# Kernel optimization log

Measured on AMD Instinct MI355X. Metric: run time of the kernel, lower is better.

Reference implementation:

```python
import jax, jax.numpy as jnp
import numpy as np

P = 16          # patch size
NUM_HEADS = 8
WINDOW = 64     # window_size from SparseAttention(window_size=64)


def _layer_norm(x, w, b, eps=1e-5):
    mu = jnp.mean(x, axis=-1, keepdims=True)
    var = jnp.var(x, axis=-1, keepdims=True)
    return (x - mu) * jax.lax.rsqrt(var + eps) * w + b


def _sinusoidal_pe(num_patches, num_features, dtype):
    pos = jnp.arange(num_patches, dtype=jnp.float32)[:, None]            # [N,1]
    i = jnp.arange(0, num_features, 2, dtype=jnp.float32)                # [D/2]
    div = jnp.exp(-jnp.log(10000.0) * i / num_features)                  # [D/2]
    ang = pos * div                                                      # [N,D/2]
    pe = jnp.stack([jnp.sin(ang), jnp.cos(ang)], axis=-1).reshape(num_patches, num_features)
    return pe.astype(dtype)


def _ffn(x, w1, b1, w2, b2):
    # FeedForward: Linear -> GELU -> Linear (dropout inactive at eval)
    h = jax.nn.gelu(jnp.einsum('bnd,hd->bnh', x, w1) + b1)
    return jnp.einsum('bnh,dh->bnd', h, w2) + b2


def _windowed_attention(x, qkv_w, qkv_b, proj_w, proj_b):
    B, N, D = x.shape
    hd = D // NUM_HEADS
    qkv = jnp.einsum('bnd,ed->bne', x, qkv_w) + qkv_b                    # [B,N,3D]
    qkv = qkv.reshape(B, N, 3, NUM_HEADS, hd)
    q, k, v = qkv[:, :, 0], qkv[:, :, 1], qkv[:, :, 2]                   # [B,N,H,hd]
    nw = N // WINDOW
    # partition sequence into non-overlapping windows of 64 tokens
    q = q.reshape(B, nw, WINDOW, NUM_HEADS, hd).transpose(0, 3, 1, 2, 4)  # [B,H,nw,W,hd]
    k = k.reshape(B, nw, WINDOW, NUM_HEADS, hd).transpose(0, 3, 1, 2, 4)
    v = v.reshape(B, nw, WINDOW, NUM_HEADS, hd).transpose(0, 3, 1, 2, 4)
    scale = 1.0 / jnp.sqrt(jnp.asarray(hd, x.dtype))
    scores = jnp.einsum('bhwqd,bhwkd->bhwqk', q, k) * scale              # [B,H,nw,W,W]
    attn = jax.nn.softmax(scores, axis=-1)
    out = jnp.einsum('bhwqk,bhwkd->bhwqd', attn, v)                      # [B,H,nw,W,hd]
    out = out.transpose(0, 2, 3, 1, 4).reshape(B, N, D)
    return jnp.einsum('bnd,ed->bne', out, proj_w) + proj_b


def setup_inputs() -> dict:
    key = jax.random.key(0)
    ks = jax.random.split(key, 8)
    D, HF = 256, 1024
    s = lambda fan: 1.0 / np.sqrt(fan)
    return {
        'x': jax.random.normal(ks[0], (32, 3, 512, 512), jnp.float32),
        'conv_w': jax.random.normal(ks[1], (D, 3, P, P), jnp.float32) * s(3 * P * P),
        'conv_b': jnp.zeros((D,), jnp.float32),
        'ln_w': jnp.ones((D,), jnp.float32),
        'ln_b': jnp.zeros((D,), jnp.float32),
        'qkv_w': jax.random.normal(ks[2], (3 * D, D), jnp.float32) * s(D),
        'qkv_b': jnp.zeros((3 * D,), jnp.float32),
        'proj_w': jax.random.normal(ks[3], (D, D), jnp.float32) * s(D),
        'proj_b': jnp.zeros((D,), jnp.float32),
        'ff_w1': jax.random.normal(ks[4], (HF, D), jnp.float32) * s(D),
        'ff_b1': jnp.zeros((HF,), jnp.float32),
        'ff_w2': jax.random.normal(ks[5], (D, HF), jnp.float32) * s(HF),
        'ff_b2': jnp.zeros((D,), jnp.float32),
    }


def reference(x, conv_w, conv_b, ln_w, ln_b, qkv_w, qkv_b, proj_w, proj_b,
              ff_w1, ff_b1, ff_w2, ff_b2):
    B, C, H, W = x.shape
    D = conv_w.shape[0]
    # PatchEmbedding1: Conv2d(C, D, kernel=16, stride=16) == per-patch matmul, then LayerNorm
    nH, nW = H // P, W // P
    patches = x.reshape(B, C, nH, P, nW, P).transpose(0, 2, 4, 1, 3, 5).reshape(B, nH * nW, C * P * P)
    h = jnp.einsum('bnp,dp->bnd', patches, conv_w.reshape(D, -1)) + conv_b
    h = _layer_norm(h, ln_w, ln_b)
    # static sinusoidal position embedding
    h = h + _sinusoidal_pe(h.shape[1], D, h.dtype)
    # block 1: FFN -> sparse (windowed) attention -> residual
    identity = h
    h = _ffn(h, ff_w1, ff_b1, ff_w2, ff_b2)
    h = _windowed_attention(h, qkv_w, qkv_b, proj_w, proj_b)
    h = h + identity
    # block 2: shared FFN -> residual
    identity = h
    h = _ffn(h, ff_w1, ff_b1, ff_w2, ff_b2)
    return h + identity
```

## Files before the change

kernel.cpp:

```cpp
#include <hip/hip_runtime.h>
#include <math.h>


#define M_TOK 32768

typedef __attribute__((ext_vector_type(8))) short  short8;
typedef __attribute__((ext_vector_type(4))) float  f32x4;
typedef __attribute__((ext_vector_type(8))) unsigned short us8v;
typedef __attribute__((ext_vector_type(4))) unsigned short us4v;

__device__ __forceinline__ unsigned short f2b(float f) {
    union { float f; unsigned u; } c; c.f = f;
    unsigned r = c.u + 0x7fffu + ((c.u >> 16) & 1u);
    return (unsigned short)(r >> 16);
}
__device__ __forceinline__ float gelu_fast(float x) {
    const float c0 = 0.7978845608028654f;
    const float c1 = 0.044715f * 0.7978845608028654f;
    float z = x * (c0 + c1 * x * x);
    float e = __expf(-2.0f * z);
    return x * __builtin_amdgcn_rcpf(1.0f + e);
}
__device__ __forceinline__ void load_lds16(const unsigned short* g, void* lds) {
    __builtin_amdgcn_global_load_lds(
        (const __attribute__((address_space(1))) unsigned int*)g,
        (__attribute__((address_space(3))) unsigned int*)lds, 16, 0, 0);
}

__global__ __launch_bounds__(256) void cvt_f2b_kernel(
    const float* __restrict__ in, unsigned short* __restrict__ out, int n)
{
    int i = (blockIdx.x * 256 + threadIdx.x) * 4;
    if (i >= n) return;
    float4 v = *(const float4*)(in + i);
    us4v o;
    o[0] = f2b(v.x); o[1] = f2b(v.y); o[2] = f2b(v.z); o[3] = f2b(v.w);
    *(us4v*)(out + i) = o;
}

__global__ __launch_bounds__(256) void cvt_weights_kernel(
    const float* __restrict__ s0, const float* __restrict__ s1,
    const float* __restrict__ s2, const float* __restrict__ s3,
    const float* __restrict__ s4,
    unsigned short* __restrict__ d0, unsigned short* __restrict__ d1,
    unsigned short* __restrict__ d2, unsigned short* __restrict__ d3,
    unsigned short* __restrict__ d4)
{
    const int bid = blockIdx.x;
    const float* src; unsigned short* dst; int off;
    if      (bid < 192) { src = s0; dst = d0; off = bid; }
    else if (bid < 384) { src = s1; dst = d1; off = bid - 192; }
    else if (bid < 448) { src = s2; dst = d2; off = bid - 384; }
    else if (bid < 704) { src = s3; dst = d3; off = bid - 448; }
    else                { src = s4; dst = d4; off = bid - 704; }
    const int i = off * 1024 + threadIdx.x * 4;
    float4 v = *(const float4*)(src + i);
    us4v o;
    o[0] = f2b(v.x); o[1] = f2b(v.y); o[2] = f2b(v.z); o[3] = f2b(v.w);
    *(us4v*)(dst + i) = o;
}

__global__ __launch_bounds__(256) void pe_init_kernel(float* __restrict__ pe)
{
    const int pos = blockIdx.x;
    const int d   = threadIdx.x;
    const int ieven = d & ~1;
    float div = expf(-9.210340371976184f * (float)ieven * (1.0f / 256.0f));
    float ang = (float)pos * div;
    pe[pos * 256 + d] = (d & 1) ? cosf(ang) : sinf(ang);
}

template<bool GELU, bool RES, bool WF32, bool WB16>
__global__ __launch_bounds__(512) void mfma_gemm_kernel(
    const unsigned short* __restrict__ A, const unsigned short* __restrict__ W,
    const float* __restrict__ bias, const float* __restrict__ res,
    float* __restrict__ outF, unsigned short* __restrict__ outB,
    int M, int N, int K)
{
    __shared__ unsigned short As[2 * 128 * 64];
    __shared__ unsigned short Ws[2 * 128 * 64];

    const int t    = threadIdx.x;
    const int m0   = blockIdx.x * 128;
    const int n0   = blockIdx.y * 128;
    const int wv   = t >> 6, lane = t & 63;
    const int wr   = (wv >> 2) * 64;
    const int wc   = (wv & 3) * 32;
    const int l15  = lane & 15, quad = lane >> 4;

    f32x4 acc[4][2];
#pragma unroll
    for (int i = 0; i < 4; i++)
#pragma unroll
        for (int j = 0; j < 2; j++)
#pragma unroll
            for (int r = 0; r < 4; r++) acc[i][j][r] = 0.0f;

    const int srow = wv * 8 + (lane >> 3);
    const int skk  = (((lane & 7) ^ ((lane >> 3) & 7)) * 8);
    const unsigned short* gA = A + (size_t)(m0 + srow) * K + skk;
    const unsigned short* gW = W + (size_t)(n0 + srow) * K + skk;
    char* lA = (char*)As + wv * 1024;
    char* lW = (char*)Ws + wv * 1024;

    const int cswz = (l15 & 7) * 8;
    const int nt   = K >> 6;

#define GSTAGE(tt, BUFOFF)                                                     \
    {                                                                          \
        const int kk = (tt) << 6;                                              \
        _Pragma("unroll")                                                      \
        for (int s = 0; s < 2; s++) {                                          \
            load_lds16(gA + (size_t)(s * 64) * K + kk, lA + (BUFOFF) + s * 8192); \
            load_lds16(gW + (size_t)(s * 64) * K + kk, lW + (BUFOFF) + s * 8192); \
        }                                                                      \
    }

#define GCOMPUTE(BUFOFF)                                                       \
    {                                                                          \
        const unsigned short* Ab = (const unsigned short*)((const char*)As + (BUFOFF)); \
        const unsigned short* Wb = (const unsigned short*)((const char*)Ws + (BUFOFF)); \
        _Pragma("unroll")                                                      \
        for (int kh = 0; kh < 2; kh++) {                                       \
            const int coff = (kh * 32 + quad * 8) ^ cswz;                      \
            short8 af[4], wf[2];                                               \
            _Pragma("unroll")                                                  \
            for (int i = 0; i < 4; i++)                                        \
                af[i] = *(const short8*)&Ab[(wr + i * 16 + l15) * 64 + coff];  \
            _Pragma("unroll")                                                  \
            for (int j = 0; j < 2; j++)                                        \
                wf[j] = *(const short8*)&Wb[(wc + j * 16 + l15) * 64 + coff];  \
            _Pragma("unroll")                                                  \
            for (int i = 0; i < 4; i++)                                        \
                _Pragma("unroll")                                              \
                for (int j = 0; j < 2; j++)                                    \
                    acc[i][j] = __builtin_amdgcn_mfma_f32_16x16x32_bf16(       \
                        af[i], wf[j], acc[i][j], 0, 0, 0);                     \
        }                                                                      \
    }

    GSTAGE(0, 0);
    for (int tt = 0; tt < nt; tt += 2) {
        GSTAGE(tt + 1, 16384);
        asm volatile("s_waitcnt vmcnt(4)" ::: "memory");
        __builtin_amdgcn_s_barrier();
        __builtin_amdgcn_sched_barrier(0);
        GCOMPUTE(0);
        __builtin_amdgcn_s_barrier();
        if (tt + 2 < nt) {
            GSTAGE(tt + 2, 0);
            asm volatile("s_waitcnt vmcnt(4)" ::: "memory");
        } else {
            asm volatile("s_waitcnt vmcnt(0)" ::: "memory");
        }
        __builtin_amdgcn_s_barrier();
        __builtin_amdgcn_sched_barrier(0);
        GCOMPUTE(16384);
        __builtin_amdgcn_s_barrier();
    }
#undef GSTAGE
#undef GCOMPUTE

#pragma unroll
    for (int i = 0; i < 4; i++) {
        const int gr = m0 + wr + i * 16 + quad * 4;
#pragma unroll
        for (int j = 0; j < 2; j++) {
            const int gc = n0 + wc + j * 16 + l15;
            const float bv = bias[gc];
#pragma unroll
            for (int r = 0; r < 4; r++) {
                float v = acc[i][j][r] + bv;
                if (GELU) v = gelu_fast(v);
                if (RES)  v += res[(size_t)(gr + r) * N + gc];
                if (WF32) outF[(size_t)(gr + r) * N + gc] = v;
                if (WB16) outB[(size_t)(gr + r) * N + gc] = f2b(v);
            }
        }
    }
}

__global__ __launch_bounds__(512) void patch_mfma_kernel(
    const unsigned short* __restrict__ xb, const unsigned short* __restrict__ W,
    const float* __restrict__ bias, float* __restrict__ outF)
{
    __shared__ unsigned short As[2 * 128 * 64];
    __shared__ unsigned short Ws[2 * 128 * 64];

    const int t    = threadIdx.x;
    const int m0   = blockIdx.x * 128;
    const int n0   = blockIdx.y * 128;
    const int wv   = t >> 6, lane = t & 63;
    const int wr   = (wv >> 2) * 64;
    const int wc   = (wv & 3) * 32;
    const int l15  = lane & 15, quad = lane >> 4;

    f32x4 acc[4][2];
#pragma unroll
    for (int i = 0; i < 4; i++)
#pragma unroll
        for (int j = 0; j < 2; j++)
#pragma unroll
            for (int r = 0; r < 4; r++) acc[i][j][r] = 0.0f;

    const int srow = wv * 8 + (lane >> 3);
    const int skk  = (((lane & 7) ^ ((lane >> 3) & 7)) * 8);
    size_t xoff[2];
#pragma unroll
    for (int s = 0; s < 2; s++) {
        const int m  = m0 + s * 64 + srow;
        const int b  = m >> 10;
        const int idx = m & 1023;
        const int hh = idx >> 5, ww = idx & 31;
        xoff[s] = ((size_t)(b * 3) * 512 + (size_t)(hh * 16)) * 512 + ww * 16;
    }
    const unsigned short* gW = W + (size_t)(n0 + srow) * 768 + skk;
    char* lA = (char*)As + wv * 1024;
    char* lW = (char*)Ws + wv * 1024;

    const int cswz = (l15 & 7) * 8;

#define PSTAGE(tt, BUFOFF)                                                     \
    {                                                                          \
        const int kk = ((tt) << 6) + skk;    \
        const int c  = kk >> 8;                                                \
        const int ph = (kk >> 4) & 15;                                         \
        const int pw = kk & 15;                                                \
        const size_t koff = (size_t)c * 262144 + (size_t)ph * 512 + pw;        \
        _Pragma("unroll")                                                      \
        for (int s = 0; s < 2; s++) {                                          \
            load_lds16(xb + xoff[s] + koff, lA + (BUFOFF) + s * 8192);         \
            load_lds16(gW + (size_t)(s * 64) * 768 + ((tt) << 6),              \
                       lW + (BUFOFF) + s * 8192);                              \
        }                                                                      \
    }

#define PCOMPUTE(BUFOFF)                                                       \
    {                                                                          \
        const unsigned short* Ab = (const unsigned short*)((const char*)As + (BUFOFF)); \
        const unsigned short* Wb = (const unsigned short*)((const char*)Ws + (BUFOFF)); \
        _Pragma("unroll")                                                      \
        for (int kh = 0; kh < 2; kh++) {                                       \
            const int coff = (kh * 32 + quad * 8) ^ cswz;                      \
            short8 af[4], wf[2];                                               \
            _Pragma("unroll")                                                  \
            for (int i = 0; i < 4; i++)                                        \
                af[i] = *(const short8*)&Ab[(wr + i * 16 + l15) * 64 + coff];  \
            _Pragma("unroll")                                                  \
            for (int j = 0; j < 2; j++)                                        \
                wf[j] = *(const short8*)&Wb[(wc + j * 16 + l15) * 64 + coff];  \
            _Pragma("unroll")                                                  \
            for (int i = 0; i < 4; i++)                                        \
                _Pragma("unroll")                                              \
                for (int j = 0; j < 2; j++)                                    \
                    acc[i][j] = __builtin_amdgcn_mfma_f32_16x16x32_bf16(       \
                        af[i], wf[j], acc[i][j], 0, 0, 0);                     \
        }                                                                      \
    }

    PSTAGE(0, 0);
    for (int tt = 0; tt < 12; tt += 2) {
        PSTAGE(tt + 1, 16384);
        asm volatile("s_waitcnt vmcnt(4)" ::: "memory");
        __builtin_amdgcn_s_barrier();
        __builtin_amdgcn_sched_barrier(0);
        PCOMPUTE(0);
        __builtin_amdgcn_s_barrier();
        if (tt + 2 < 12) {
            PSTAGE(tt + 2, 0);
            asm volatile("s_waitcnt vmcnt(4)" ::: "memory");
        } else {
            asm volatile("s_waitcnt vmcnt(0)" ::: "memory");
        }
        __builtin_amdgcn_s_barrier();
        __builtin_amdgcn_sched_barrier(0);
        PCOMPUTE(16384);
        __builtin_amdgcn_s_barrier();
    }
#undef PSTAGE
#undef PCOMPUTE

#pragma unroll
    for (int i = 0; i < 4; i++) {
        const int gr = m0 + wr + i * 16 + quad * 4;
#pragma unroll
        for (int j = 0; j < 2; j++) {
            const int gc = n0 + wc + j * 16 + l15;
            const float bv = bias[gc];
#pragma unroll
            for (int r = 0; r < 4; r++)
                outF[(size_t)(gr + r) * 256 + gc] = acc[i][j][r] + bv;
        }
    }
}

__global__ __launch_bounds__(256) void ln_pe_kernel(
    const float* __restrict__ in, const float* __restrict__ w,
    const float* __restrict__ b, const float* __restrict__ pe_t,
    float* __restrict__ outF, unsigned short* __restrict__ outB)
{
    const int m = blockIdx.x;
    const int d = threadIdx.x;
    float v = in[(size_t)m * 256 + d];

    float s = v, s2 = v * v;
#pragma unroll
    for (int off = 32; off > 0; off >>= 1) {
        s  += __shfl_down(s,  off, 64);
        s2 += __shfl_down(s2, off, 64);
    }
    __shared__ float ss[4], ss2[4], stats[2];
    const int lane = d & 63, wid = d >> 6;
    if (lane == 0) { ss[wid] = s; ss2[wid] = s2; }
    __syncthreads();
    if (d == 0) {
        float a  = ss[0] + ss[1] + ss[2] + ss[3];
        float a2 = ss2[0] + ss2[1] + ss2[2] + ss2[3];
        float mean = a * (1.0f / 256.0f);
        float var  = a2 * (1.0f / 256.0f) - mean * mean;
        stats[0] = mean;
        stats[1] = rsqrtf(var + 1e-5f);
    }
    __syncthreads();
    const float mean = stats[0], rstd = stats[1];

    const int pos = m & 1023;
    float pe = pe_t[pos * 256 + d];

    float o = (v - mean) * rstd * w[d] + b[d] + pe;
    outF[(size_t)m * 256 + d] = o;
    outB[(size_t)m * 256 + d] = f2b(o);
}

__global__ __launch_bounds__(256) void attn_mfma_kernel(
    const unsigned short* __restrict__ qkv, unsigned short* __restrict__ out)
{
    __shared__ unsigned short Ps[64 * 72];
    __shared__ unsigned short Vt[32 * 72];

    const int blk = blockIdx.x;
    const int h = blk & 7;
    const int w = (blk >> 3) & 15;
    const int b = blk >> 7;
    const int m_base = b * 1024 + w * 64;

    const int t = threadIdx.x;
    const int wv = t >> 6, lane = t & 63;
    const int l15 = lane & 15, quad = lane >> 4;

    {
        const int row = t >> 2;
        const int c0  = (t & 3) * 8;
        const unsigned short* src = qkv + (size_t)(m_base + row) * 768 + 512 + h * 32 + c0;
        us8v v = *(const us8v*)src;
#pragma unroll
        for (int j = 0; j < 8; j++) Vt[(c0 + j) * 72 + row] = v[j];
    }

    short8 aq = *(const short8*)(qkv + (size_t)(m_base + wv * 16 + l15) * 768 + h * 32 + quad * 8);
    f32x4 c[4];
#pragma unroll
    for (int j = 0; j < 4; j++) {
        short8 bk = *(const short8*)(qkv + (size_t)(m_base + j * 16 + l15) * 768 + 256 + h * 32 + quad * 8);
        f32x4 z = {0.0f, 0.0f, 0.0f, 0.0f};
        c[j] = __builtin_amdgcn_mfma_f32_16x16x32_bf16(aq, bk, z, 0, 0, 0);
    }

    const float scale = 0.17677669529663687f;
    float sm[4];
#pragma unroll
    for (int r = 0; r < 4; r++) {
        float m0 = -1e30f;
#pragma unroll
        for (int j = 0; j < 4; j++) { c[j][r] *= scale; m0 = fmaxf(m0, c[j][r]); }
#pragma unroll
        for (int d = 1; d < 16; d <<= 1) m0 = fmaxf(m0, __shfl_xor(m0, d, 64));
        float s0 = 0.0f;
#pragma unroll
        for (int j = 0; j < 4; j++) { float e = __expf(c[j][r] - m0); c[j][r] = e; s0 += e; }
#pragma unroll
        for (int d = 1; d < 16; d <<= 1) s0 += __shfl_xor(s0, d, 64);
        sm[r] = __builtin_amdgcn_rcpf(s0);
    }

#pragma unroll
    for (int r = 0; r < 4; r++) {
        const int prow = wv * 16 + quad * 4 + r;
#pragma unroll
        for (int j = 0; j < 4; j++)
            Ps[prow * 72 + j * 16 + l15] = f2b(c[j][r] * sm[r]);
    }
    __syncthreads();

    short8 ap0 = *(const short8*)&Ps[(wv * 16 + l15) * 72 + quad * 8];
    short8 ap1 = *(const short8*)&Ps[(wv * 16 + l15) * 72 + 32 + quad * 8];
    f32x4 o[2];
#pragma unroll
    for (int nt = 0; nt < 2; nt++) {
        short8 bv0 = *(const short8*)&Vt[(nt * 16 + l15) * 72 + quad * 8];
        short8 bv1 = *(const short8*)&Vt[(nt * 16 + l15) * 72 + 32 + quad * 8];
        f32x4 z = {0.0f, 0.0f, 0.0f, 0.0f};
        o[nt] = __builtin_amdgcn_mfma_f32_16x16x32_bf16(ap0, bv0, z, 0, 0, 0);
        o[nt] = __builtin_amdgcn_mfma_f32_16x16x32_bf16(ap1, bv1, o[nt], 0, 0, 0);
    }

#pragma unroll
    for (int nt = 0; nt < 2; nt++) {
#pragma unroll
        for (int r = 0; r < 4; r++) {
            const int row = m_base + wv * 16 + quad * 4 + r;
            out[(size_t)row * 256 + h * 32 + nt * 16 + l15] = f2b(o[nt][r]);
        }
    }
}

extern "C" void kernel_launch(void* const* d_in, const int* in_sizes, int n_in,
                              void* d_out, int out_size, void* d_ws, size_t ws_size,
                              hipStream_t stream)
{
    const float* x      = (const float*)d_in[0];
    const float* conv_w = (const float*)d_in[1];
    const float* conv_b = (const float*)d_in[2];
    const float* ln_w   = (const float*)d_in[3];
    const float* ln_b   = (const float*)d_in[4];
    const float* qkv_w  = (const float*)d_in[5];
    const float* qkv_b  = (const float*)d_in[6];
    const float* proj_w = (const float*)d_in[7];
    const float* proj_b = (const float*)d_in[8];
    const float* ff_w1  = (const float*)d_in[9];
    const float* ff_b1  = (const float*)d_in[10];
    const float* ff_w2  = (const float*)d_in[11];
    const float* ff_b2  = (const float*)d_in[12];
    float* out = (float*)d_out;

    char* ws = (char*)d_ws;
    unsigned short* xb    = (unsigned short*)(ws);
    unsigned short* hidb  = (unsigned short*)(ws);
    float*          h0    = (float*)(ws + 67108864);
    unsigned short* qkvb  = (unsigned short*)(ws + 67108864);
    float*          pe_t  = (float*)(ws + 100663296);
    float*          h1f   = (float*)(ws + 117440512);
    unsigned short* h1b   = (unsigned short*)(ws + 150994944);
    unsigned short* aob   = (unsigned short*)(ws + 150994944);
    unsigned short* f1b   = (unsigned short*)(ws + 167772160);
    unsigned short* h2b   = (unsigned short*)(ws + 167772160);
    unsigned short* wbase = (unsigned short*)(ws + 184549376);
    unsigned short* conv_wb = wbase;
    unsigned short* qkv_wb  = wbase + 196608;
    unsigned short* proj_wb = wbase + 393216;
    unsigned short* ff_w1b  = wbase + 458752;
    unsigned short* ff_w2b  = wbase + 720896;

    const int M = M_TOK;
    dim3 blk(256);
    dim3 blk512(512);

    cvt_f2b_kernel<<<dim3(25165824 / 1024), blk, 0, stream>>>(x, xb, 25165824);
    cvt_weights_kernel<<<dim3(960), blk, 0, stream>>>(
        conv_w, qkv_w, proj_w, ff_w1, ff_w2,
        conv_wb, qkv_wb, proj_wb, ff_w1b, ff_w2b);
    pe_init_kernel<<<dim3(1024), blk, 0, stream>>>(pe_t);

    patch_mfma_kernel<<<dim3(M / 128, 2), blk512, 0, stream>>>(xb, conv_wb, conv_b, h0);
    ln_pe_kernel<<<dim3(M), blk, 0, stream>>>(h0, ln_w, ln_b, pe_t, h1f, h1b);
    mfma_gemm_kernel<true, false, false, true><<<dim3(M / 128, 8), blk512, 0, stream>>>(
        h1b, ff_w1b, ff_b1, nullptr, nullptr, hidb, M, 1024, 256);
    mfma_gemm_kernel<false, false, false, true><<<dim3(M / 128, 2), blk512, 0, stream>>>(
        hidb, ff_w2b, ff_b2, nullptr, nullptr, f1b, M, 256, 1024);
    mfma_gemm_kernel<false, false, false, true><<<dim3(M / 128, 6), blk512, 0, stream>>>(
        f1b, qkv_wb, qkv_b, nullptr, nullptr, qkvb, M, 768, 256);
    attn_mfma_kernel<<<dim3(4096), blk, 0, stream>>>(qkvb, aob);
    mfma_gemm_kernel<false, true, true, true><<<dim3(M / 128, 2), blk512, 0, stream>>>(
        aob, proj_wb, proj_b, h1f, out, h2b, M, 256, 256);
    mfma_gemm_kernel<true, false, false, true><<<dim3(M / 128, 8), blk512, 0, stream>>>(
        h2b, ff_w1b, ff_b1, nullptr, nullptr, hidb, M, 1024, 256);
    mfma_gemm_kernel<false, true, true, false><<<dim3(M / 128, 2), blk512, 0, stream>>>(
        hidb, ff_w2b, ff_b2, out, out, nullptr, M, 256, 1024);
}
```

Measured before the change: 394.3 us.

## Fuse fp32-to-bf16 input conversion into patch-embedding GEMM with full-N tile

Removes the separate kernel that converted the 100MB fp32 image to bf16. The patch GEMM now loads fp32 pixels directly through registers, converts them and writes swizzled bf16 into LDS. Each block covers all 256 output features (N=256), so every image tile is read once instead of twice. The cost is a register-staged A path in place of the direct global-to-LDS loads, more accumulators per wave, and double the weight LDS.

```diff
diff --git a/kernel.cpp b/kernel.cpp
--- a/kernel.cpp
+++ b/kernel.cpp
@@ -25,17 +25,6 @@
     __builtin_amdgcn_global_load_lds(
         (const __attribute__((address_space(1))) unsigned int*)g,
         (__attribute__((address_space(3))) unsigned int*)lds, 16, 0, 0);
-}
-
-__global__ __launch_bounds__(256) void cvt_f2b_kernel(
-    const float* __restrict__ in, unsigned short* __restrict__ out, int n)
-{
-    int i = (blockIdx.x * 256 + threadIdx.x) * 4;
-    if (i >= n) return;
-    float4 v = *(const float4*)(in + i);
-    us4v o;
-    o[0] = f2b(v.x); o[1] = f2b(v.y); o[2] = f2b(v.z); o[3] = f2b(v.w);
-    *(us4v*)(out + i) = o;
 }
 
 __global__ __launch_bounds__(256) void cvt_weights_kernel(
@@ -180,112 +169,134 @@
     }
 }
 
-__global__ __launch_bounds__(512) void patch_mfma_kernel(
-    const unsigned short* __restrict__ xb, const unsigned short* __restrict__ W,
+__global__ __launch_bounds__(512) void patch_fused_kernel(
+    const float* __restrict__ x, const unsigned short* __restrict__ W,
     const float* __restrict__ bias, float* __restrict__ outF)
 {
     __shared__ unsigned short As[2 * 128 * 64];
-    __shared__ unsigned short Ws[2 * 128 * 64];
+    __shared__ unsigned short Ws[2 * 256 * 64];
 
     const int t    = threadIdx.x;
     const int m0   = blockIdx.x * 128;
-    const int n0   = blockIdx.y * 128;
     const int wv   = t >> 6, lane = t & 63;
     const int wr   = (wv >> 2) * 64;
-    const int wc   = (wv & 3) * 32;
+    const int wc   = (wv & 3) * 64;
     const int l15  = lane & 15, quad = lane >> 4;
 
-    f32x4 acc[4][2];
+    f32x4 acc[4][4];
 #pragma unroll
     for (int i = 0; i < 4; i++)
 #pragma unroll
-        for (int j = 0; j < 2; j++)
+        for (int j = 0; j < 4; j++)
 #pragma unroll
             for (int r = 0; r < 4; r++) acc[i][j][r] = 0.0f;
 
-    const int srow = wv * 8 + (lane >> 3);
-    const int skk  = (((lane & 7) ^ ((lane >> 3) & 7)) * 8);
-    size_t xoff[2];
-#pragma unroll
-    for (int s = 0; s < 2; s++) {
-        const int m  = m0 + s * 64 + srow;
-        const int b  = m >> 10;
-        const int idx = m & 1023;
-        const int hh = idx >> 5, ww = idx & 31;
-        xoff[s] = ((size_t)(b * 3) * 512 + (size_t)(hh * 16)) * 512 + ww * 16;
-    }
-    const unsigned short* gW = W + (size_t)(n0 + srow) * 768 + skk;
-    char* lA = (char*)As + wv * 1024;
+    const int ar  = t >> 2;
+    const int ac0 = (t & 3) * 16;
+    const int am  = m0 + ar;
+    const int ab  = am >> 10;
+    const int ahh = (am >> 5) & 31;
+    const int aww = am & 31;
+    const float* axbase = x + (size_t)ab * 786432 + (size_t)ahh * 8192 + aww * 16;
+    const int alc = ac0 >> 3;
+    char* aw0 = (char*)As + ar * 128 + ((alc    ) ^ (ar & 7)) * 16;
+    char* aw1 = (char*)As + ar * 128 + ((alc + 1) ^ (ar & 7)) * 16;
+
+    const int wsrow = wv * 8 + (lane >> 3);
+    const int wskk  = (((lane & 7) ^ ((lane >> 3) & 7)) * 8);
+    const unsigned short* gW = W + (size_t)wsrow * 768 + wskk;
     char* lW = (char*)Ws + wv * 1024;
 
     const int cswz = (l15 & 7) * 8;
 
-#define PSTAGE(tt, BUFOFF)                                                     \
-    {                                                                          \
-        const int kk = ((tt) << 6) + skk;    \
-        const int c  = kk >> 8;                                                \
-        const int ph = (kk >> 4) & 15;                                         \
-        const int pw = kk & 15;                                                \
-        const size_t koff = (size_t)c * 262144 + (size_t)ph * 512 + pw;        \
+    float4 av0, av1, av2, av3;
+
+#define PA_ISSUE(tt)                                                           \
+    {                                                                          \
+        const int k0 = ((tt) << 6) + ac0;                                      \
+        const int c  = k0 >> 8;                                                \
+        const int ph = (k0 >> 4) & 15;                                         \
+        const float* s = axbase + (size_t)c * 262144 + ph * 512;               \
+        av0 = *(const float4*)(s);                                             \
+        av1 = *(const float4*)(s + 4);                                         \
+        av2 = *(const float4*)(s + 8);                                         \
+        av3 = *(const float4*)(s + 12);                                        \
+    }
+#define PA_WRITE(BUFOFF)                                                       \
+    {                                                                          \
+        us8v o0, o1;                                                           \
+        o0[0] = f2b(av0.x); o0[1] = f2b(av0.y); o0[2] = f2b(av0.z); o0[3] = f2b(av0.w); \
+        o0[4] = f2b(av1.x); o0[5] = f2b(av1.y); o0[6] = f2b(av1.z); o0[7] = f2b(av1.w); \
+        o1[0] = f2b(av2.x); o1[1] = f2b(av2.y); o1[2] = f2b(av2.z); o1[3] = f2b(av2.w); \
+        o1[4] = f2b(av3.x); o1[5] = f2b(av3.y); o1[6] = f2b(av3.z); o1[7] = f2b(av3.w); \
+        *(us8v*)(aw0 + (BUFOFF)) = o0;                                         \
+        *(us8v*)(aw1 + (BUFOFF)) = o1;                                         \
+    }
+#define PW_ISSUE(tt, BUFOFF)                                                   \
+    {                                                                          \
+        const int kk = (tt) << 6;                                              \
         _Pragma("unroll")                                                      \
-        for (int s = 0; s < 2; s++) {                                          \
-            load_lds16(xb + xoff[s] + koff, lA + (BUFOFF) + s * 8192);         \
-            load_lds16(gW + (size_t)(s * 64) * 768 + ((tt) << 6),              \
-                       lW + (BUFOFF) + s * 8192);                              \
-        }                                                                      \
-    }
-
-#define PCOMPUTE(BUFOFF)                                                       \
-    {                                                                          \
-        const unsigned short* Ab = (const unsigned short*)((const char*)As + (BUFOFF)); \
-        const unsigned short* Wb = (const unsigned short*)((const char*)Ws + (BUFOFF)); \
+        for (int s = 0; s < 4; s++)                                            \
+            load_lds16(gW + (size_t)(s * 64) * 768 + kk, lW + (BUFOFF) + s * 8192); \
+    }
+#define PCOMPUTE(AOFF, WOFF)                                                   \
+    {                                                                          \
+        const unsigned short* Ab = (const unsigned short*)((const char*)As + (AOFF)); \
+        const unsigned short* Wb = (const unsigned short*)((const char*)Ws + (WOFF)); \
         _Pragma("unroll")                                                      \
         for (int kh = 0; kh < 2; kh++) {                                       \
             const int coff = (kh * 32 + quad * 8) ^ cswz;                      \
-            short8 af[4], wf[2];                                               \
+            short8 af[4], wf[4];                                               \
             _Pragma("unroll")                                                  \
             for (int i = 0; i < 4; i++)                                        \
                 af[i] = *(const short8*)&Ab[(wr + i * 16 + l15) * 64 + coff];  \
             _Pragma("unroll")                                                  \
-            for (int j = 0; j < 2; j++)                                        \
+            for (int j = 0; j < 4; j++)                                        \
                 wf[j] = *(const short8*)&Wb[(wc + j * 16 + l15) * 64 + coff];  \
             _Pragma("unroll")                                                  \
             for (int i = 0; i < 4; i++)                                        \
                 _Pragma("unroll")                                              \
-                for (int j = 0; j < 2; j++)                                    \
+                for (int j = 0; j < 4; j++)                                    \
                     acc[i][j] = __builtin_amdgcn_mfma_f32_16x16x32_bf16(       \
                         af[i], wf[j], acc[i][j], 0, 0, 0);                     \
         }                                                                      \
     }
 
-    PSTAGE(0, 0);
-    for (int tt = 0; tt < 12; tt += 2) {
-        PSTAGE(tt + 1, 16384);
-        asm volatile("s_waitcnt vmcnt(4)" ::: "memory");
-        __builtin_amdgcn_s_barrier();
-        __builtin_amdgcn_sched_barrier(0);
-        PCOMPUTE(0);
-        __builtin_amdgcn_s_barrier();
-        if (tt + 2 < 12) {
-            PSTAGE(tt + 2, 0);
-            asm volatile("s_waitcnt vmcnt(4)" ::: "memory");
-        } else {
+    PA_ISSUE(0);
+    PW_ISSUE(0, 0);
+    asm volatile("s_waitcnt vmcnt(0)" ::: "memory");
+    PA_WRITE(0);
+    asm volatile("s_waitcnt lgkmcnt(0)" ::: "memory");
+    __builtin_amdgcn_s_barrier();
+    __builtin_amdgcn_sched_barrier(0);
+
+    for (int tt = 0; tt < 12; ++tt) {
+        const int aoff_c = (tt & 1) * 16384;
+        const int woff_c = (tt & 1) * 32768;
+        if (tt < 11) {
+            PA_ISSUE(tt + 1);
+            PW_ISSUE(tt + 1, woff_c ^ 32768);
+        }
+        PCOMPUTE(aoff_c, woff_c);
+        if (tt < 11) {
             asm volatile("s_waitcnt vmcnt(0)" ::: "memory");
-        }
-        __builtin_amdgcn_s_barrier();
-        __builtin_amdgcn_sched_barrier(0);
-        PCOMPUTE(16384);
-        __builtin_amdgcn_s_barrier();
-    }
-#undef PSTAGE
+            PA_WRITE(aoff_c ^ 16384);
+            asm volatile("s_waitcnt lgkmcnt(0)" ::: "memory");
+            __builtin_amdgcn_s_barrier();
+            __builtin_amdgcn_sched_barrier(0);
+        }
+    }
+#undef PA_ISSUE
+#undef PA_WRITE
+#undef PW_ISSUE
 #undef PCOMPUTE
 
 #pragma unroll
     for (int i = 0; i < 4; i++) {
         const int gr = m0 + wr + i * 16 + quad * 4;
 #pragma unroll
-        for (int j = 0; j < 2; j++) {
-            const int gc = n0 + wc + j * 16 + l15;
+        for (int j = 0; j < 4; j++) {
+            const int gc = wc + j * 16 + l15;
             const float bv = bias[gc];
 #pragma unroll
             for (int r = 0; r < 4; r++)
@@ -434,7 +445,6 @@
     float* out = (float*)d_out;
 
     char* ws = (char*)d_ws;
-    unsigned short* xb    = (unsigned short*)(ws);
     unsigned short* hidb  = (unsigned short*)(ws);
     float*          h0    = (float*)(ws + 67108864);
     unsigned short* qkvb  = (unsigned short*)(ws + 67108864);
@@ -455,13 +465,12 @@
     dim3 blk(256);
     dim3 blk512(512);
 
-    cvt_f2b_kernel<<<dim3(25165824 / 1024), blk, 0, stream>>>(x, xb, 25165824);
     cvt_weights_kernel<<<dim3(960), blk, 0, stream>>>(
         conv_w, qkv_w, proj_w, ff_w1, ff_w2,
         conv_wb, qkv_wb, proj_wb, ff_w1b, ff_w2b);
     pe_init_kernel<<<dim3(1024), blk, 0, stream>>>(pe_t);
 
-    patch_mfma_kernel<<<dim3(M / 128, 2), blk512, 0, stream>>>(xb, conv_wb, conv_b, h0);
+    patch_fused_kernel<<<dim3(M / 128), blk512, 0, stream>>>(x, conv_wb, conv_b, h0);
     ln_pe_kernel<<<dim3(M), blk, 0, stream>>>(h0, ln_w, ln_b, pe_t, h1f, h1b);
     mfma_gemm_kernel<true, false, false, true><<<dim3(M / 128, 8), blk512, 0, stream>>>(
         h1b, ff_w1b, ff_b1, nullptr, nullptr, hidb, M, 1024, 256);
```

Result: no change. 389.0 us (-1.4%).
